# Performance work log

Hardware: AMD Instinct MI355X
Metric: run time of the kernel (lower is better)

The kernel has to match this reference:

```python
import jax, jax.numpy as jnp
import numpy as np

B, L, H, HS, OUT = 4, 512, 768, 64, 16  # batch, seq_len, hidden, head_size, output_size


def setup_inputs() -> dict:
    key = jax.random.key(0)
    ks = jax.random.split(key, 4)
    return {
        "x": jax.random.normal(ks[0], (B, L, H), dtype=jnp.float32),
        "Wq": jax.random.normal(ks[1], (H, HS), dtype=jnp.float32) * 0.02,
        "bq": jnp.zeros((HS,), dtype=jnp.float32),
        "Wk": jax.random.normal(ks[2], (H, HS), dtype=jnp.float32) * 0.02,
        "bk": jnp.zeros((HS,), dtype=jnp.float32),
        "Wb": jax.random.normal(ks[3], (4 * HS, OUT), dtype=jnp.float32) * 0.02,
        "bb": jnp.zeros((OUT,), dtype=jnp.float32),
    }


def _tri_indices(seq_len):
    # pair p corresponds to (start=i, end=j) with j >= i, ordered by i then j
    idx_start = np.repeat(np.arange(seq_len), np.arange(seq_len, 0, -1))
    idx_end = np.concatenate([np.arange(i, seq_len) for i in range(seq_len)])
    return idx_start, idx_end


def reference(x, Wq, bq, Wk, bk, Wb, bb):
    seq_len = x.shape[1]
    idx_start, idx_end = _tri_indices(seq_len)  # static numpy, P = L*(L+1)/2

    # Project per-token first (math-equivalent to projecting the gathered
    # pair tensors, since Linear is applied token-wise), then gather pairs.
    q = x @ Wq + bq  # [B, L, HS]
    k = x @ Wk + bk  # [B, L, HS]

    q_start = q[:, idx_start]  # query(start_token_hidden)  [B, P, HS]
    q_end = q[:, idx_end]      # query(end_token_hidden)
    k_end = k[:, idx_end]      # key(end_token_hidden) == key_start == key_end

    # entity_type_bias(cat([query_start, key_start, query_end, key_end]))
    feat = jnp.concatenate([q_start, k_end, q_end, k_end], axis=-1) @ Wb + bb  # [B, P, OUT]

    # einsum('blnh,blnh->bln') with n=1 -> per-pair dot product, broadcast over OUT
    score = jnp.einsum('bph,bph->bp', q_start, k_end)[..., None]  # [B, P, 1]
    return score + feat  # [B, P, OUT]
```

## Files before the change

kernel.cpp:

```cpp
#include <hip/hip_runtime.h>

#define Bc   4
#define Lc   512
#define Hc   768
#define HSc  64
#define OUTc 16
#define Pc   131328
#define NTOK 2048
#define XPITCH 776

typedef float  floatx4 __attribute__((ext_vector_type(4)));
typedef short  bf16x8  __attribute__((ext_vector_type(8)));
typedef float  f32x4   __attribute__((ext_vector_type(4)));


__device__ __forceinline__ unsigned short f2bf(float f) {
    unsigned int u = __float_as_uint(f);
    return (unsigned short)((u + 0x7FFFu + ((u >> 16) & 1u)) >> 16);
}

__global__ __launch_bounds__(256) void qkae_kernel(
    const float* __restrict__ x, const float* __restrict__ Wq,
    const float* __restrict__ Wk, const float* __restrict__ bq,
    const float* __restrict__ bk, const float* __restrict__ Wb,
    const float* __restrict__ bb,
    float* __restrict__ qws, float* __restrict__ kws,
    float* __restrict__ Aws, float* __restrict__ Eqws,
    float* __restrict__ Ekws)
{
    __shared__ alignas(16) unsigned short xs[16 * XPITCH];
    __shared__ float lw0[64 * OUTc];
    __shared__ float lw1[64 * OUTc];
    __shared__ float lqk[16][64];

    const int tid  = threadIdx.x;
    const int mb   = blockIdx.x >> 1;
    const int half = blockIdx.x & 1;
    const int m0   = mb * 16;

    if (half == 0) {
        #pragma unroll
        for (int i = 0; i < 4; ++i) {
            lw0[tid + i * 256] = Wb[tid + i * 256];
            lw1[tid + i * 256] = Wb[2048 + tid + i * 256];
        }
    } else {
        #pragma unroll
        for (int i = 0; i < 4; ++i) {
            lw0[tid + i * 256] = Wb[1024 + tid + i * 256] + Wb[3072 + tid + i * 256];
        }
    }

    {
        const float4* xg = (const float4*)(x + (size_t)m0 * Hc);
        #pragma unroll
        for (int i = 0; i < 12; ++i) {
            const int idx = tid + i * 256;
            const int r   = idx / 192;
            const int c4  = idx - r * 192;
            const float4 v = xg[idx];
            *(ushort4*)(xs + r * XPITCH + c4 * 4) =
                make_ushort4(f2bf(v.x), f2bf(v.y), f2bf(v.z), f2bf(v.w));
        }
    }
    __syncthreads();

    const int w    = tid >> 6;
    const int lane = tid & 63;
    const int l15  = lane & 15;
    const int quad = lane >> 4;
    const int nq   = w * 16 + l15;

    const float* bsrc = half ? Wk : Wq;
    const unsigned short* ap = xs + l15 * XPITCH + quad * 8;

    f32x4 acc = {0.f, 0.f, 0.f, 0.f};
    #pragma unroll 4
    for (int k0 = 0; k0 < Hc; k0 += 32) {
        const bf16x8 af = *(const bf16x8*)(ap + k0);
        const int kb = k0 + quad * 8;
        bf16x8 bf;
        #pragma unroll
        for (int j = 0; j < 8; ++j)
            bf[j] = (short)f2bf(bsrc[(kb + j) * HSc + nq]);
        acc = __builtin_amdgcn_mfma_f32_16x16x32_bf16(af, bf, acc, 0, 0, 0);
    }

    const float bias = half ? bk[nq] : bq[nq];
    float* dst = half ? kws : qws;
    #pragma unroll
    for (int r = 0; r < 4; ++r) {
        const int t = quad * 4 + r;
        const float v = acc[r] + bias;
        dst[(size_t)(m0 + t) * HSc + nq] = v;
        lqk[t][nq] = v;
    }
    __syncthreads();

    const int t   = tid >> 4;
    const int c   = tid & 15;
    const int tok = m0 + t;
    const float* row = lqk[t];
    if (half == 0) {
        float a = 0.f, eq = 0.f;
        #pragma unroll 8
        for (int h = 0; h < 64; ++h) {
            const float rv = row[h];
            a  += rv * lw0[h * OUTc + c];
            eq += rv * lw1[h * OUTc + c];
        }
        Aws[(size_t)tok * OUTc + c]  = a;
        Eqws[(size_t)tok * OUTc + c] = eq;
    } else {
        float ek = bb[c];
        #pragma unroll 8
        for (int h = 0; h < 64; ++h)
            ek += row[h] * lw0[h * OUTc + c];
        Ekws[(size_t)tok * OUTc + c] = ek;
    }
}

__global__ __launch_bounds__(256) void pair_kernel(
    const float* __restrict__ qws, const float* __restrict__ kws,
    const float* __restrict__ Aws, const float* __restrict__ Eqws,
    const float* __restrict__ Ekws,
    float* __restrict__ out)
{
    int n = blockIdx.x;
    int g = 0;
    int cnt = 32;
    while (n >= cnt) { n -= cnt; ++g; cnt = 4 * (8 - g); }
    const int span = 8 - g;
    const int i = g * 4 + n / span;
    const int j = g + n % span;
    const int b = blockIdx.y;

    __shared__ alignas(16) float q_tile[16][64];
    __shared__ alignas(16) float A_tile[16][16];

    const int tid = threadIdx.x;
    const int s0 = i * 16;
    const int e0 = j * 64;

    {
        const int r = tid >> 4, c4 = tid & 15;
        ((float4*)q_tile[r])[c4] =
            ((const float4*)(qws + ((size_t)b * Lc + s0 + r) * HSc))[c4];
        if (tid < 64) {
            const int ra = tid >> 2, ca = tid & 3;
            ((float4*)A_tile[ra])[ca] =
                ((const float4*)(Aws + ((size_t)b * Lc + s0 + ra) * OUTc))[ca];
        }
    }
    __syncthreads();

    const int gidx = tid >> 2;
    const int l = tid & 3;
    const int e = e0 + gidx;

    const float4* kk = (const float4*)(kws + ((size_t)b * Lc + e) * HSc);
    const float4 kv0 = kk[l];
    const float4 kv1 = kk[4 + l];
    const float4 kv2 = kk[8 + l];
    const float4 kv3 = kk[12 + l];
    const float4 evq = ((const float4*)(Eqws + ((size_t)b * Lc + e) * OUTc))[l];
    const float4 evk = ((const float4*)(Ekws + ((size_t)b * Lc + e) * OUTc))[l];
    const float4 ev  = make_float4(evq.x + evk.x, evq.y + evk.y,
                                   evq.z + evk.z, evq.w + evk.w);

    float* ob = out + (size_t)b * Pc * OUTc;

    #pragma unroll 8
    for (int sl = 0; sl < 16; ++sl) {
        const int s = s0 + sl;
        const float4* qq = (const float4*)q_tile[sl];
        const float4 qv0 = qq[l];
        const float4 qv1 = qq[4 + l];
        const float4 qv2 = qq[8 + l];
        const float4 qv3 = qq[12 + l];

        float sc = qv0.x * kv0.x + qv0.y * kv0.y + qv0.z * kv0.z + qv0.w * kv0.w
                 + qv1.x * kv1.x + qv1.y * kv1.y + qv1.z * kv1.z + qv1.w * kv1.w
                 + qv2.x * kv2.x + qv2.y * kv2.y + qv2.z * kv2.z + qv2.w * kv2.w
                 + qv3.x * kv3.x + qv3.y * kv3.y + qv3.z * kv3.z + qv3.w * kv3.w;
        sc += __shfl_xor(sc, 1);
        sc += __shfl_xor(sc, 2);

        if (e >= s) {
            const float4 av = ((const float4*)A_tile[sl])[l];
            const int row = s * (2 * Lc + 1 - s) / 2 + (e - s);
            floatx4 r;
            r.x = av.x + ev.x + sc;
            r.y = av.y + ev.y + sc;
            r.z = av.z + ev.z + sc;
            r.w = av.w + ev.w + sc;
            __builtin_nontemporal_store(r, (floatx4*)(ob + (size_t)row * OUTc) + l);
        }
    }
}

extern "C" void kernel_launch(void* const* d_in, const int* in_sizes, int n_in,
                              void* d_out, int out_size, void* d_ws, size_t ws_size,
                              hipStream_t stream) {
    const float* x  = (const float*)d_in[0];
    const float* Wq = (const float*)d_in[1];
    const float* bq = (const float*)d_in[2];
    const float* Wk = (const float*)d_in[3];
    const float* bk = (const float*)d_in[4];
    const float* Wb = (const float*)d_in[5];
    const float* bb = (const float*)d_in[6];

    float* ws   = (float*)d_ws;
    float* qws  = ws;
    float* kws  = ws + 131072;
    float* Aws  = ws + 262144;
    float* Eqws = ws + 294912;
    float* Ekws = ws + 327680;

    qkae_kernel<<<dim3(256), dim3(256), 0, stream>>>(
        x, Wq, Wk, bq, bk, Wb, bb, qws, kws, Aws, Eqws, Ekws);
    pair_kernel<<<dim3(144, 4), dim3(256), 0, stream>>>(
        qws, kws, Aws, Eqws, Ekws, (float*)d_out);
}
```

Baseline: 90.64 us.

## Fuse projection and pair kernels with per-block release/acquire flags

```diff
diff --git a/kernel.cpp b/kernel.cpp
--- a/kernel.cpp
+++ b/kernel.cpp
@@ -19,182 +19,204 @@
     return (unsigned short)((u + 0x7FFFu + ((u >> 16) & 1u)) >> 16);
 }
 
-__global__ __launch_bounds__(256) void qkae_kernel(
+__global__ __launch_bounds__(256, 3) void fused_kernel(
     const float* __restrict__ x, const float* __restrict__ Wq,
     const float* __restrict__ Wk, const float* __restrict__ bq,
     const float* __restrict__ bk, const float* __restrict__ Wb,
     const float* __restrict__ bb,
     float* __restrict__ qws, float* __restrict__ kws,
     float* __restrict__ Aws, float* __restrict__ Eqws,
-    float* __restrict__ Ekws)
-{
-    __shared__ alignas(16) unsigned short xs[16 * XPITCH];
-    __shared__ float lw0[64 * OUTc];
-    __shared__ float lw1[64 * OUTc];
-    __shared__ float lqk[16][64];
-
-    const int tid  = threadIdx.x;
-    const int mb   = blockIdx.x >> 1;
-    const int half = blockIdx.x & 1;
-    const int m0   = mb * 16;
-
-    if (half == 0) {
-        #pragma unroll
-        for (int i = 0; i < 4; ++i) {
-            lw0[tid + i * 256] = Wb[tid + i * 256];
-            lw1[tid + i * 256] = Wb[2048 + tid + i * 256];
-        }
-    } else {
-        #pragma unroll
-        for (int i = 0; i < 4; ++i) {
-            lw0[tid + i * 256] = Wb[1024 + tid + i * 256] + Wb[3072 + tid + i * 256];
-        }
-    }
-
-    {
-        const float4* xg = (const float4*)(x + (size_t)m0 * Hc);
-        #pragma unroll
-        for (int i = 0; i < 12; ++i) {
-            const int idx = tid + i * 256;
-            const int r   = idx / 192;
-            const int c4  = idx - r * 192;
-            const float4 v = xg[idx];
-            *(ushort4*)(xs + r * XPITCH + c4 * 4) =
-                make_ushort4(f2bf(v.x), f2bf(v.y), f2bf(v.z), f2bf(v.w));
-        }
-    }
-    __syncthreads();
-
-    const int w    = tid >> 6;
-    const int lane = tid & 63;
-    const int l15  = lane & 15;
-    const int quad = lane >> 4;
-    const int nq   = w * 16 + l15;
-
-    const float* bsrc = half ? Wk : Wq;
-    const unsigned short* ap = xs + l15 * XPITCH + quad * 8;
-
-    f32x4 acc = {0.f, 0.f, 0.f, 0.f};
-    #pragma unroll 4
-    for (int k0 = 0; k0 < Hc; k0 += 32) {
-        const bf16x8 af = *(const bf16x8*)(ap + k0);
-        const int kb = k0 + quad * 8;
-        bf16x8 bf;
-        #pragma unroll
-        for (int j = 0; j < 8; ++j)
-            bf[j] = (short)f2bf(bsrc[(kb + j) * HSc + nq]);
-        acc = __builtin_amdgcn_mfma_f32_16x16x32_bf16(af, bf, acc, 0, 0, 0);
-    }
-
-    const float bias = half ? bk[nq] : bq[nq];
-    float* dst = half ? kws : qws;
-    #pragma unroll
-    for (int r = 0; r < 4; ++r) {
-        const int t = quad * 4 + r;
-        const float v = acc[r] + bias;
-        dst[(size_t)(m0 + t) * HSc + nq] = v;
-        lqk[t][nq] = v;
-    }
-    __syncthreads();
-
-    const int t   = tid >> 4;
-    const int c   = tid & 15;
-    const int tok = m0 + t;
-    const float* row = lqk[t];
-    if (half == 0) {
-        float a = 0.f, eq = 0.f;
-        #pragma unroll 8
-        for (int h = 0; h < 64; ++h) {
-            const float rv = row[h];
-            a  += rv * lw0[h * OUTc + c];
-            eq += rv * lw1[h * OUTc + c];
-        }
-        Aws[(size_t)tok * OUTc + c]  = a;
-        Eqws[(size_t)tok * OUTc + c] = eq;
-    } else {
-        float ek = bb[c];
-        #pragma unroll 8
-        for (int h = 0; h < 64; ++h)
-            ek += row[h] * lw0[h * OUTc + c];
-        Ekws[(size_t)tok * OUTc + c] = ek;
-    }
-}
-
-__global__ __launch_bounds__(256) void pair_kernel(
-    const float* __restrict__ qws, const float* __restrict__ kws,
-    const float* __restrict__ Aws, const float* __restrict__ Eqws,
-    const float* __restrict__ Ekws,
+    float* __restrict__ Ekws, unsigned* __restrict__ flags,
     float* __restrict__ out)
 {
-    int n = blockIdx.x;
-    int g = 0;
-    int cnt = 32;
-    while (n >= cnt) { n -= cnt; ++g; cnt = 4 * (8 - g); }
-    const int span = 8 - g;
-    const int i = g * 4 + n / span;
-    const int j = g + n % span;
-    const int b = blockIdx.y;
-
-    __shared__ alignas(16) float q_tile[16][64];
-    __shared__ alignas(16) float A_tile[16][16];
-
+    __shared__ alignas(16) unsigned char smem[37120];
     const int tid = threadIdx.x;
-    const int s0 = i * 16;
-    const int e0 = j * 64;
+    const int bx  = blockIdx.x;
+
+    if (bx < 256) {
+        unsigned short* xs  = (unsigned short*)smem;
+        float*          lw0 = (float*)(smem + 24832);
+        float*          lw1 = (float*)(smem + 28928);
+        float*          lqk = (float*)(smem + 33024);
+
+        const int mb   = bx >> 1;
+        const int half = bx & 1;
+        const int m0   = mb * 16;
+
+        if (half == 0) {
+            #pragma unroll
+            for (int i = 0; i < 4; ++i) {
+                lw0[tid + i * 256] = Wb[tid + i * 256];
+                lw1[tid + i * 256] = Wb[2048 + tid + i * 256];
+            }
+        } else {
+            #pragma unroll
+            for (int i = 0; i < 4; ++i) {
+                lw0[tid + i * 256] = Wb[1024 + tid + i * 256] + Wb[3072 + tid + i * 256];
+            }
+        }
+
+        {
+            const float4* xg = (const float4*)(x + (size_t)m0 * Hc);
+            #pragma unroll
+            for (int i = 0; i < 12; ++i) {
+                const int idx = tid + i * 256;
+                const int r   = idx / 192;
+                const int c4  = idx - r * 192;
+                const float4 v = xg[idx];
+                *(ushort4*)(xs + r * XPITCH + c4 * 4) =
+                    make_ushort4(f2bf(v.x), f2bf(v.y), f2bf(v.z), f2bf(v.w));
+            }
+        }
+        __syncthreads();
+
+        const int w    = tid >> 6;
+        const int lane = tid & 63;
+        const int l15  = lane & 15;
+        const int quad = lane >> 4;
+        const int nq   = w * 16 + l15;
+
+        const float* bsrc = half ? Wk : Wq;
+        const unsigned short* ap = xs + l15 * XPITCH + quad * 8;
+
+        f32x4 acc = {0.f, 0.f, 0.f, 0.f};
+        #pragma unroll 4
+        for (int k0 = 0; k0 < Hc; k0 += 32) {
+            const bf16x8 af = *(const bf16x8*)(ap + k0);
+            const int kb = k0 + quad * 8;
+            bf16x8 bf;
+            #pragma unroll
+            for (int j = 0; j < 8; ++j)
+                bf[j] = (short)f2bf(bsrc[(kb + j) * HSc + nq]);
+            acc = __builtin_amdgcn_mfma_f32_16x16x32_bf16(af, bf, acc, 0, 0, 0);
+        }
+
+        const float bias = half ? bk[nq] : bq[nq];
+        float* dst = half ? kws : qws;
+        #pragma unroll
+        for (int r = 0; r < 4; ++r) {
+            const int t = quad * 4 + r;
+            const float v = acc[r] + bias;
+            dst[(size_t)(m0 + t) * HSc + nq] = v;
+            lqk[t * 64 + nq] = v;
+        }
+        __syncthreads();
+
+        const int t   = tid >> 4;
+        const int c   = tid & 15;
+        const int tok = m0 + t;
+        const float* row = lqk + t * 64;
+        if (half == 0) {
+            float a = 0.f, eq = 0.f;
+            #pragma unroll 8
+            for (int h = 0; h < 64; ++h) {
+                const float rv = row[h];
+                a  += rv * lw0[h * OUTc + c];
+                eq += rv * lw1[h * OUTc + c];
+            }
+            Aws[(size_t)tok * OUTc + c]  = a;
+            Eqws[(size_t)tok * OUTc + c] = eq;
+        } else {
+            float ek = bb[c];
+            #pragma unroll 8
+            for (int h = 0; h < 64; ++h)
+                ek += row[h] * lw0[h * OUTc + c];
+            Ekws[(size_t)tok * OUTc + c] = ek;
+        }
+
+        __threadfence();
+        __syncthreads();
+        if (tid == 0)
+            __hip_atomic_store(&flags[bx], 1u, __ATOMIC_RELEASE,
+                               __HIP_MEMORY_SCOPE_AGENT);
+    }
 
     {
-        const int r = tid >> 4, c4 = tid & 15;
-        ((float4*)q_tile[r])[c4] =
-            ((const float4*)(qws + ((size_t)b * Lc + s0 + r) * HSc))[c4];
-        if (tid < 64) {
-            const int ra = tid >> 2, ca = tid & 3;
-            ((float4*)A_tile[ra])[ca] =
-                ((const float4*)(Aws + ((size_t)b * Lc + s0 + ra) * OUTc))[ca];
-        }
-    }
-    __syncthreads();
-
-    const int gidx = tid >> 2;
-    const int l = tid & 3;
-    const int e = e0 + gidx;
-
-    const float4* kk = (const float4*)(kws + ((size_t)b * Lc + e) * HSc);
-    const float4 kv0 = kk[l];
-    const float4 kv1 = kk[4 + l];
-    const float4 kv2 = kk[8 + l];
-    const float4 kv3 = kk[12 + l];
-    const float4 evq = ((const float4*)(Eqws + ((size_t)b * Lc + e) * OUTc))[l];
-    const float4 evk = ((const float4*)(Ekws + ((size_t)b * Lc + e) * OUTc))[l];
-    const float4 ev  = make_float4(evq.x + evk.x, evq.y + evk.y,
-                                   evq.z + evk.z, evq.w + evk.w);
-
-    float* ob = out + (size_t)b * Pc * OUTc;
-
-    #pragma unroll 8
-    for (int sl = 0; sl < 16; ++sl) {
-        const int s = s0 + sl;
-        const float4* qq = (const float4*)q_tile[sl];
-        const float4 qv0 = qq[l];
-        const float4 qv1 = qq[4 + l];
-        const float4 qv2 = qq[8 + l];
-        const float4 qv3 = qq[12 + l];
-
-        float sc = qv0.x * kv0.x + qv0.y * kv0.y + qv0.z * kv0.z + qv0.w * kv0.w
-                 + qv1.x * kv1.x + qv1.y * kv1.y + qv1.z * kv1.z + qv1.w * kv1.w
-                 + qv2.x * kv2.x + qv2.y * kv2.y + qv2.z * kv2.z + qv2.w * kv2.w
-                 + qv3.x * kv3.x + qv3.y * kv3.y + qv3.z * kv3.z + qv3.w * kv3.w;
-        sc += __shfl_xor(sc, 1);
-        sc += __shfl_xor(sc, 2);
-
-        if (e >= s) {
-            const float4 av = ((const float4*)A_tile[sl])[l];
-            const int row = s * (2 * Lc + 1 - s) / 2 + (e - s);
-            floatx4 r;
-            r.x = av.x + ev.x + sc;
-            r.y = av.y + ev.y + sc;
-            r.z = av.z + ev.z + sc;
-            r.w = av.w + ev.w + sc;
-            __builtin_nontemporal_store(r, (floatx4*)(ob + (size_t)row * OUTc) + l);
+        float* q_tile = (float*)smem;
+        float* A_tile = (float*)(smem + 4096);
+
+        int n = bx % 144;
+        const int b = bx / 144;
+        int g = 0;
+        int cnt = 32;
+        while (n >= cnt) { n -= cnt; ++g; cnt = 4 * (8 - g); }
+        const int span = 8 - g;
+        const int i = g * 4 + n / span;
+        const int j = g + n % span;
+
+        const int s0 = i * 16;
+        const int e0 = j * 64;
+
+        {
+            const int base = b * 32 + j * 4;
+            if (tid < 9) {
+                int pid;
+                if (tid == 0) pid = 2 * (b * 32 + i);
+                else {
+                    const int t = (tid - 1) & 3;
+                    pid = 2 * (base + t) + ((tid - 1) >> 2);
+                }
+                while (!__hip_atomic_load(&flags[pid], __ATOMIC_ACQUIRE,
+                                          __HIP_MEMORY_SCOPE_AGENT))
+                    __builtin_amdgcn_s_sleep(2);
+            }
+            __syncthreads();
+        }
+
+        {
+            const int r = tid >> 4, c4 = tid & 15;
+            ((float4*)(q_tile + r * 64))[c4] =
+                ((const float4*)(qws + ((size_t)b * Lc + s0 + r) * HSc))[c4];
+            if (tid < 64) {
+                const int ra = tid >> 2, ca = tid & 3;
+                ((float4*)(A_tile + ra * 16))[ca] =
+                    ((const float4*)(Aws + ((size_t)b * Lc + s0 + ra) * OUTc))[ca];
+            }
+        }
+        __syncthreads();
+
+        const int gidx = tid >> 2;
+        const int l = tid & 3;
+        const int e = e0 + gidx;
+
+        const float4* kk = (const float4*)(kws + ((size_t)b * Lc + e) * HSc);
+        const float4 kv0 = kk[l];
+        const float4 kv1 = kk[4 + l];
+        const float4 kv2 = kk[8 + l];
+        const float4 kv3 = kk[12 + l];
+        const float4 evq = ((const float4*)(Eqws + ((size_t)b * Lc + e) * OUTc))[l];
+        const float4 evk = ((const float4*)(Ekws + ((size_t)b * Lc + e) * OUTc))[l];
+        const float4 ev  = make_float4(evq.x + evk.x, evq.y + evk.y,
+                                       evq.z + evk.z, evq.w + evk.w);
+
+        float* ob = out + (size_t)b * Pc * OUTc;
+
+        #pragma unroll 8
+        for (int sl = 0; sl < 16; ++sl) {
+            const int s = s0 + sl;
+            const float4* qq = (const float4*)(q_tile + sl * 64);
+            const float4 qv0 = qq[l];
+            const float4 qv1 = qq[4 + l];
+            const float4 qv2 = qq[8 + l];
+            const float4 qv3 = qq[12 + l];
+
+            float sc = qv0.x * kv0.x + qv0.y * kv0.y + qv0.z * kv0.z + qv0.w * kv0.w
+                     + qv1.x * kv1.x + qv1.y * kv1.y + qv1.z * kv1.z + qv1.w * kv1.w
+                     + qv2.x * kv2.x + qv2.y * kv2.y + qv2.z * kv2.z + qv2.w * kv2.w
+                     + qv3.x * kv3.x + qv3.y * kv3.y + qv3.z * kv3.z + qv3.w * kv3.w;
+            sc += __shfl_xor(sc, 1);
+            sc += __shfl_xor(sc, 2);
+
+            if (e >= s) {
+                const float4 av = ((const float4*)(A_tile + sl * 16))[l];
+                const int row = s * (2 * Lc + 1 - s) / 2 + (e - s);
+                floatx4 r;
+                r.x = av.x + ev.x + sc;
+                r.y = av.y + ev.y + sc;
+                r.z = av.z + ev.z + sc;
+                r.w = av.w + ev.w + sc;
+                __builtin_nontemporal_store(r, (floatx4*)(ob + (size_t)row * OUTc) + l);
+            }
         }
     }
 }
@@ -216,9 +238,10 @@
     float* Aws  = ws + 262144;
     float* Eqws = ws + 294912;
     float* Ekws = ws + 327680;
-
-    qkae_kernel<<<dim3(256), dim3(256), 0, stream>>>(
-        x, Wq, Wk, bq, bk, Wb, bb, qws, kws, Aws, Eqws, Ekws);
-    pair_kernel<<<dim3(144, 4), dim3(256), 0, stream>>>(
-        qws, kws, Aws, Eqws, Ekws, (float*)d_out);
+    unsigned* flags = (unsigned*)(ws + 360448);
+
+    hipMemsetAsync(flags, 0, 256 * sizeof(unsigned), stream);
+    fused_kernel<<<dim3(576), dim3(256), 0, stream>>>(
+        x, Wq, Wk, bq, bk, Wb, bb, qws, kws, Aws, Eqws, Ekws, flags,
+        (float*)d_out);
 }
```

Measured after the change: 162.3 us. 79.0% more time.

## Precompute bf16 x and transposed bf16 weights in a separate prep kernel

Applied to the files above, without the earlier changes.

```diff
diff --git a/kernel.cpp b/kernel.cpp
--- a/kernel.cpp
+++ b/kernel.cpp
@@ -7,7 +7,6 @@
 #define OUTc 16
 #define Pc   131328
 #define NTOK 2048
-#define XPITCH 776
 
 typedef float  floatx4 __attribute__((ext_vector_type(4)));
 typedef short  bf16x8  __attribute__((ext_vector_type(8)));
@@ -19,16 +18,54 @@
     return (unsigned short)((u + 0x7FFFu + ((u >> 16) & 1u)) >> 16);
 }
 
+__global__ __launch_bounds__(256) void prep_kernel(
+    const float* __restrict__ x, const float* __restrict__ Wq,
+    const float* __restrict__ Wk,
+    unsigned short* __restrict__ xbf, unsigned short* __restrict__ Wt)
+{
+    const int bx  = blockIdx.x;
+    const int tid = threadIdx.x;
+    if (bx < 512) {
+        const float4* xg = (const float4*)x;
+        const int base = bx * 768;
+        #pragma unroll
+        for (int i = 0; i < 3; ++i) {
+            const int idx = base + tid + i * 256;
+            const float4 v = xg[idx];
+            ushort4 o;
+            o.x = f2bf(v.x); o.y = f2bf(v.y); o.z = f2bf(v.z); o.w = f2bf(v.w);
+            ((ushort4*)xbf)[idx] = o;
+        }
+    } else {
+        const int k0 = (bx - 512) * 16;
+        __shared__ unsigned short T[128][16];
+        const int c  = tid & 127;
+        const int kg = tid >> 7;
+        const float* Wsrc = (c < 64) ? Wq : Wk;
+        const int cc = c & 63;
+        #pragma unroll
+        for (int kk = 0; kk < 8; ++kk) {
+            const int k = k0 + kg * 8 + kk;
+            T[c][kg * 8 + kk] = f2bf(Wsrc[k * HSc + cc]);
+        }
+        __syncthreads();
+        const int n = tid >> 1;
+        const int h = tid & 1;
+        const unsigned short* src = &T[n][h * 8];
+        ushort4* dst = (ushort4*)(Wt + (size_t)n * Hc + k0 + h * 8);
+        dst[0] = make_ushort4(src[0], src[1], src[2], src[3]);
+        dst[1] = make_ushort4(src[4], src[5], src[6], src[7]);
+    }
+}
+
 __global__ __launch_bounds__(256) void qkae_kernel(
-    const float* __restrict__ x, const float* __restrict__ Wq,
-    const float* __restrict__ Wk, const float* __restrict__ bq,
-    const float* __restrict__ bk, const float* __restrict__ Wb,
-    const float* __restrict__ bb,
+    const unsigned short* __restrict__ xbf, const unsigned short* __restrict__ Wt,
+    const float* __restrict__ bq, const float* __restrict__ bk,
+    const float* __restrict__ Wb, const float* __restrict__ bb,
     float* __restrict__ qws, float* __restrict__ kws,
     float* __restrict__ Aws, float* __restrict__ Eqws,
     float* __restrict__ Ekws)
 {
-    __shared__ alignas(16) unsigned short xs[16 * XPITCH];
     __shared__ float lw0[64 * OUTc];
     __shared__ float lw1[64 * OUTc];
     __shared__ float lqk[16][64];
@@ -50,20 +87,6 @@
             lw0[tid + i * 256] = Wb[1024 + tid + i * 256] + Wb[3072 + tid + i * 256];
         }
     }
-
-    {
-        const float4* xg = (const float4*)(x + (size_t)m0 * Hc);
-        #pragma unroll
-        for (int i = 0; i < 12; ++i) {
-            const int idx = tid + i * 256;
-            const int r   = idx / 192;
-            const int c4  = idx - r * 192;
-            const float4 v = xg[idx];
-            *(ushort4*)(xs + r * XPITCH + c4 * 4) =
-                make_ushort4(f2bf(v.x), f2bf(v.y), f2bf(v.z), f2bf(v.w));
-        }
-    }
-    __syncthreads();
 
     const int w    = tid >> 6;
     const int lane = tid & 63;
@@ -71,19 +94,15 @@
     const int quad = lane >> 4;
     const int nq   = w * 16 + l15;
 
-    const float* bsrc = half ? Wk : Wq;
-    const unsigned short* ap = xs + l15 * XPITCH + quad * 8;
+    const unsigned short* ap = xbf + (size_t)(m0 + l15) * Hc + quad * 8;
+    const unsigned short* bp = Wt  + (size_t)(half * 64 + nq) * Hc + quad * 8;
 
     f32x4 acc = {0.f, 0.f, 0.f, 0.f};
-    #pragma unroll 4
+    #pragma unroll
     for (int k0 = 0; k0 < Hc; k0 += 32) {
-        const bf16x8 af = *(const bf16x8*)(ap + k0);
-        const int kb = k0 + quad * 8;
-        bf16x8 bf;
-        #pragma unroll
-        for (int j = 0; j < 8; ++j)
-            bf[j] = (short)f2bf(bsrc[(kb + j) * HSc + nq]);
-        acc = __builtin_amdgcn_mfma_f32_16x16x32_bf16(af, bf, acc, 0, 0, 0);
+        const bf16x8 a = *(const bf16x8*)(ap + k0);
+        const bf16x8 b = *(const bf16x8*)(bp + k0);
+        acc = __builtin_amdgcn_mfma_f32_16x16x32_bf16(a, b, acc, 0, 0, 0);
     }
 
     const float bias = half ? bk[nq] : bq[nq];
@@ -216,9 +235,12 @@
     float* Aws  = ws + 262144;
     float* Eqws = ws + 294912;
     float* Ekws = ws + 327680;
-
+    unsigned short* xbf = (unsigned short*)(ws + 360448);
+    unsigned short* Wt  = xbf + (size_t)NTOK * Hc;
+
+    prep_kernel<<<dim3(560), dim3(256), 0, stream>>>(x, Wq, Wk, xbf, Wt);
     qkae_kernel<<<dim3(256), dim3(256), 0, stream>>>(
-        x, Wq, Wk, bq, bk, Wb, bb, qws, kws, Aws, Eqws, Ekws);
+        xbf, Wt, bq, bk, Wb, bb, qws, kws, Aws, Eqws, Ekws);
     pair_kernel<<<dim3(144, 4), dim3(256), 0, stream>>>(
         qws, kws, Aws, Eqws, Ekws, (float*)d_out);
 }
```

Result: slower. 93.76 us (+3.4%).
